# Kernel optimization log

Hardware: AMD Instinct MI355X
Metric: run time of the kernel (lower is better)

The kernel has to match this reference:

```python
import jax, jax.numpy as jnp
import numpy as np

N_NODES = 100000
N_EDGES = 3200000
D_IN = 128
D_HID = 128
N_CLASSES = 40


def setup_inputs() -> dict:
    key = jax.random.key(0)
    ks = jax.random.split(key, 8)
    x = jax.random.normal(ks[0], (N_NODES, D_IN), dtype=jnp.float32)
    edge_index = jax.random.randint(ks[1], (2, N_EDGES), 0, N_NODES, dtype=jnp.int64)
    s1 = 1.0 / np.sqrt(D_IN)
    s2 = 1.0 / np.sqrt(D_HID)
    W1 = jax.random.normal(ks[2], (D_IN, D_HID), dtype=jnp.float32) * s1
    b1 = jnp.zeros((D_HID,), dtype=jnp.float32)
    W2 = jax.random.normal(ks[3], (D_HID, D_HID), dtype=jnp.float32) * s2
    b2 = jnp.zeros((D_HID,), dtype=jnp.float32)
    Wl = jax.random.normal(ks[4], (D_HID, N_CLASSES), dtype=jnp.float32) * s2
    bl = jnp.zeros((N_CLASSES,), dtype=jnp.float32)
    return {"x": x, "edge_index": edge_index, "W1": W1, "b1": b1,
            "W2": W2, "b2": b2, "Wl": Wl, "bl": bl}


def _gcn_conv(x, W, b, src, dst, inv_sqrt_deg, n_nodes):
    # h = X @ W  (linear transform first: cheaper when out_dim <= in_dim)
    h = x @ W  # [N, d_out]
    # symmetric normalization: norm_e = deg(src)^-1/2 * deg(dst)^-1/2
    norm = inv_sqrt_deg[src] * inv_sqrt_deg[dst]  # [E]
    msg = h[src] * norm[:, None]                  # gather + scale  [E, d_out]
    out = jax.ops.segment_sum(msg, dst, num_segments=n_nodes)  # scatter-add
    return out + b


def reference(x, edge_index, W1, b1, W2, b2, Wl, bl):
    n = x.shape[0]
    # GCNConv adds self-loops before normalization (PyG default)
    loops = jnp.arange(n, dtype=edge_index.dtype)
    src = jnp.concatenate([edge_index[0], loops])
    dst = jnp.concatenate([edge_index[1], loops])
    deg = jax.ops.segment_sum(jnp.ones_like(dst, dtype=x.dtype), dst, num_segments=n)
    inv_sqrt_deg = jnp.where(deg > 0, jax.lax.rsqrt(deg), 0.0)

    h = _gcn_conv(x, W1, b1, src, dst, inv_sqrt_deg, n)
    h = jax.nn.relu(h)
    h = _gcn_conv(h, W2, b2, src, dst, inv_sqrt_deg, n)
    h = jax.nn.relu(h)
    return h @ Wl + bl
```

## Files before the change

### kernel.cpp

```cpp
#include <hip/hip_runtime.h>
#include <hip/hip_bf16.h>

typedef _Float16 f16;
typedef _Float16 f16x4 __attribute__((ext_vector_type(4)));
typedef _Float16 f16x8 __attribute__((ext_vector_type(8)));
typedef float f32x4 __attribute__((ext_vector_type(4)));

#define D 128
#define N_CLS 40
#define BN 128
#define NBMAX 1024


__global__ __launch_bounds__(256) void k_hist(const int* __restrict__ dst,
                                              int* __restrict__ bcnt, int e) {
  __shared__ int lh[NBMAX];
  for (int j = threadIdx.x; j < NBMAX; j += 256) lh[j] = 0;
  __syncthreads();
  int stride = gridDim.x * blockDim.x;
  for (int q = blockIdx.x * blockDim.x + threadIdx.x; q < e; q += stride)
    atomicAdd(&lh[dst[q] >> 7], 1);
  __syncthreads();
  for (int j = threadIdx.x; j < NBMAX; j += 256)
    if (lh[j]) atomicAdd(&bcnt[j], lh[j]);
}

__global__ __launch_bounds__(1024) void k_bscan(const int* __restrict__ bcnt,
                                                int* __restrict__ bbase,
                                                int* __restrict__ bcur) {
  __shared__ int sums[NBMAX];
  int t = threadIdx.x;
  int c = bcnt[t];
  sums[t] = c;
  __syncthreads();
  for (int off = 1; off < NBMAX; off <<= 1) {
    int a = (t >= off) ? sums[t - off] : 0;
    __syncthreads();
    sums[t] += a;
    __syncthreads();
  }
  bbase[t] = sums[t] - c;
  bcur[t] = sums[t] - c;
}

__global__ __launch_bounds__(256) void k_place(const int* __restrict__ src,
                                               const int* __restrict__ dst,
                                               int* __restrict__ bcur,
                                               unsigned int* __restrict__ binned,
                                               int e, int nwg) {
  __shared__ int lh[NBMAX];
  __shared__ int lofs[NBMAX];
  __shared__ int lcur[NBMAX];
  int chunk = (e + nwg - 1) / nwg;
  int lo = blockIdx.x * chunk;
  int hi = min(e, lo + chunk);
  int t = threadIdx.x;
  for (int j = t; j < NBMAX; j += 256) { lh[j] = 0; lcur[j] = 0; }
  __syncthreads();
  for (int q = lo + t; q < hi; q += 256) atomicAdd(&lh[dst[q] >> 7], 1);
  __syncthreads();
  for (int j = t; j < NBMAX; j += 256) {
    int c = lh[j];
    lofs[j] = c ? atomicAdd(&bcur[j], c) : 0;
  }
  __syncthreads();
  for (int q = lo + t; q < hi; q += 256) {
    int d = dst[q];
    int b = d >> 7;
    int r = atomicAdd(&lcur[b], 1);
    binned[lofs[b] + r] = ((unsigned int)(d & 127) << 17) | (unsigned int)src[q];
  }
}

__global__ __launch_bounds__(256) void k_csr(const unsigned int* __restrict__ binned,
                                             const int* __restrict__ bbase,
                                             int* __restrict__ csr,
                                             int* __restrict__ deg,
                                             float* __restrict__ isd,
                                             int* __restrict__ row_start, int n) {
  int b = blockIdx.x;
  int lo = bbase[b], hi = bbase[b + 1];
  __shared__ int h[BN];
  __shared__ int sc[BN];
  __shared__ int cur[BN];
  int t = threadIdx.x;
  if (t < BN) h[t] = 0;
  __syncthreads();
  for (int q = lo + t; q < hi; q += 256) atomicAdd(&h[binned[q] >> 17], 1);
  __syncthreads();
  if (t < BN) sc[t] = h[t];
  __syncthreads();
  for (int off = 1; off < BN; off <<= 1) {
    int a = 0;
    if (t < BN && t >= off) a = sc[t - off];
    __syncthreads();
    if (t < BN) sc[t] += a;
    __syncthreads();
  }
  if (t < BN) {
    int excl = sc[t] - h[t];
    cur[t] = lo + excl;
    int i = b * BN + t;
    if (i < n) {
      deg[i] = h[t];
      isd[i] = rsqrtf((float)(h[t] + 1));
      row_start[i] = lo + excl;
    }
  }
  __syncthreads();
  for (int q = lo + t; q < hi; q += 256) {
    unsigned int u = binned[q];
    int p = atomicAdd(&cur[u >> 17], 1);
    csr[p] = (int)(u & 0x1FFFF);
  }
}

template <bool HALF_IN>
__global__ __launch_bounds__(256) void k_gemm_m(const void* __restrict__ Xv,
                                                const float* __restrict__ W,
                                                const float* __restrict__ isd,
                                                f16* __restrict__ HS, int n) {
  __shared__ f16 At[64][136];
  __shared__ f16 Wt[128][136];
  const size_t ss = (size_t)n * 16;
  int t = threadIdx.x;
  int r0 = blockIdx.x * 64;
  if (!HALF_IN) {
    const float* X = (const float*)Xv;
    for (int q = t; q < 64 * 32; q += 256) {
      int row = q >> 5, cb = (q & 31) << 2;
      float4 v = {0.f, 0.f, 0.f, 0.f};
      if (r0 + row < n) v = *(const float4*)(X + (size_t)(r0 + row) * D + cb);
      f16x4 h = {(f16)v.x, (f16)v.y, (f16)v.z, (f16)v.w};
      *(f16x4*)&At[row][cb] = h;
    }
  } else {
    const f16* X = (const f16*)Xv;
    for (int q = t; q < 64 * 16; q += 256) {
      int row = q >> 4, cb = (q & 15) << 3;
      f16x8 v = 0;
      if (r0 + row < n) v = *(const f16x8*)(X + (size_t)(r0 + row) * D + cb);
      *(f16x8*)&At[row][cb] = v;
    }
  }
  for (int q = t; q < D * D; q += 256) {
    int k = q >> 7, c = q & 127;
    Wt[c][k] = (f16)W[q];
  }
  __syncthreads();

  int wave = t >> 6, lane = t & 63;
  int lw = lane & 15, kg = lane >> 4;
  f32x4 acc[8];
#pragma unroll
  for (int ct = 0; ct < 8; ++ct) acc[ct] = (f32x4)0.f;
#pragma unroll
  for (int ks = 0; ks < 4; ++ks) {
    f16x8 af = *(const f16x8*)&At[(wave << 4) + lw][ks * 32 + kg * 8];
#pragma unroll
    for (int ct = 0; ct < 8; ++ct) {
      f16x8 bf = *(const f16x8*)&Wt[ct * 16 + lw][ks * 32 + kg * 8];
      acc[ct] = __builtin_amdgcn_mfma_f32_16x16x32_f16(af, bf, acc[ct], 0, 0, 0);
    }
  }
  int rbase = r0 + (wave << 4) + (kg << 2);
  float sv[4];
#pragma unroll
  for (int rr = 0; rr < 4; ++rr)
    sv[rr] = (rbase + rr < n) ? isd[rbase + rr] : 0.f;
#pragma unroll
  for (int ct = 0; ct < 8; ++ct) {
#pragma unroll
    for (int rr = 0; rr < 4; ++rr) {
      int node = rbase + rr;
      if (node < n)
        HS[(size_t)ct * ss + (size_t)node * 16 + lw] = (f16)(acc[ct][rr] * sv[rr]);
    }
  }
}

__device__ inline f16x8 shfl_xor_f16x8(f16x8 v, int m) {
  union { f16x8 h; int i[4]; } u;
  u.h = v;
#pragma unroll
  for (int k = 0; k < 4; ++k) u.i[k] = __shfl_xor(u.i[k], m);
  return u.h;
}

__global__ __launch_bounds__(256) void k_aggs(const f16* __restrict__ HS,
                                              const int* __restrict__ csr,
                                              const int* __restrict__ row_start,
                                              const int* __restrict__ deg,
                                              const float* __restrict__ bias,
                                              f16* __restrict__ G, int n) {
  const size_t ss = (size_t)n * 16;
  int t = threadIdx.x;
  int wave = t >> 6, lane = t & 63;
  int g = lane >> 4, r = lane & 15;
  int s = blockIdx.x & 7;
  int i0 = ((blockIdx.x >> 3) << 4) + (wave << 2) + g;
  bool ok = i0 < n;
  int i = ok ? i0 : n - 1;
  int hf = r & 1, er = r >> 1;
  int dg = deg[i];
  const int* cp = csr + row_start[i];
  const char* sbase = (const char*)(HS + (size_t)s * ss);
  unsigned hofs = (unsigned)(hf << 4);
  f16x8 a0 = (f16x8)0, a1 = (f16x8)0;
  int iA = cp[er];
  int iB = cp[er + 8];
  for (int u = 0; u < dg; u += 16) {
    unsigned oA = ((unsigned)iA << 5) + hofs;
    unsigned oB = ((unsigned)iB << 5) + hofs;
    iA = cp[u + 16 + er];
    iB = cp[u + 24 + er];
    if (u + er < dg)
      a0 += *(const f16x8*)(sbase + oA);
    if (u + 8 + er < dg)
      a1 += *(const f16x8*)(sbase + oB);
  }
  f16x8 tv = a0 + a1;
  tv += shfl_xor_f16x8(tv, 2);
  tv += shfl_xor_f16x8(tv, 4);
  tv += shfl_xor_f16x8(tv, 8);
  f16x8 svv = *(const f16x8*)(sbase + ((unsigned)i << 5) + hofs);
  float di = rsqrtf((float)(dg + 1));
  const float* bp = bias + s * 16 + (hf << 3);
  float4 b0 = *(const float4*)bp;
  float4 b1 = *(const float4*)(bp + 4);
  float bv[8] = {b0.x, b0.y, b0.z, b0.w, b1.x, b1.y, b1.z, b1.w};
  f16x8 ov;
#pragma unroll
  for (int j = 0; j < 8; ++j) {
    float v = di * ((float)tv[j] + (float)svv[j]) + bv[j];
    v = v > 0.f ? v : 0.f;
    ov[j] = (f16)v;
  }
  if (ok && r < 2)
    *(f16x8*)(G + (size_t)i * D + s * 16 + (hf << 3)) = ov;
}

__global__ __launch_bounds__(256) void k_cls(const f16* __restrict__ H,
                                             const float* __restrict__ Wl,
                                             const float* __restrict__ bl,
                                             float* __restrict__ out, int n) {
  __shared__ float wt[N_CLS][D];
  int t = threadIdx.x;
  for (int q = t; q < D * N_CLS; q += 256) {
    int k = q / N_CLS, c = q - k * N_CLS;
    wt[c][k] = Wl[q];
  }
  int wv = t >> 6, lane = t & 63, g = lane >> 4, l = lane & 15;
  float bb0 = bl[l];
  float bb1 = bl[16 + l];
  float bb2 = (l < 8) ? bl[32 + l] : 0.f;
  __syncthreads();
  int node0 = (blockIdx.x << 7) + (wv << 2) + g;
  for (int it = 0; it < 8; ++it) {
    int node = node0 + it * 16;
    if (node >= n) break;
    f16x8 h = *(const f16x8*)(H + (size_t)node * D + l * 8);
    float hf[8];
#pragma unroll
    for (int j = 0; j < 8; ++j) hf[j] = (float)h[j];
    float r0 = bb0, r1 = bb1, r2 = bb2;
#pragma unroll 4
    for (int c = 0; c < N_CLS; ++c) {
      const float* wp = &wt[c][l * 8];
      float4 w0 = *(const float4*)wp;
      float4 w1 = *(const float4*)(wp + 4);
      float p = hf[0] * w0.x + hf[1] * w0.y + hf[2] * w0.z + hf[3] * w0.w +
                hf[4] * w1.x + hf[5] * w1.y + hf[6] * w1.z + hf[7] * w1.w;
      p += __shfl_xor(p, 1);
      p += __shfl_xor(p, 2);
      p += __shfl_xor(p, 4);
      p += __shfl_xor(p, 8);
      if ((c & 15) == l) {
        if (c < 16) r0 += p;
        else if (c < 32) r1 += p;
        else r2 += p;
      }
    }
    float* op = out + (size_t)node * N_CLS;
    op[l] = r0;
    op[16 + l] = r1;
    if (l < 8) op[32 + l] = r2;
  }
}

extern "C" void kernel_launch(void* const* d_in, const int* in_sizes, int n_in,
                              void* d_out, int out_size, void* d_ws, size_t ws_size,
                              hipStream_t stream) {
  const float* x  = (const float*)d_in[0];
  const int*   ei = (const int*)d_in[1];
  const float* W1 = (const float*)d_in[2];
  const float* b1 = (const float*)d_in[3];
  const float* W2 = (const float*)d_in[4];
  const float* b2 = (const float*)d_in[5];
  const float* Wl = (const float*)d_in[6];
  const float* bl = (const float*)d_in[7];
  float* out = (float*)d_out;

  const int n = in_sizes[0] / D;
  const int e = in_sizes[1] / 2;
  const int* src = ei;
  const int* dst = ei + e;
  const int nb = (n + BN - 1) / BN;

  char* ws = (char*)d_ws;
  size_t off = 0;
  auto alloc = [&](size_t bytes) -> void* {
    void* p = ws + off;
    off += (bytes + 255) & ~(size_t)255;
    return p;
  };
  int*   bcnt      = (int*)alloc(NBMAX * 4);
  int*   bbase     = (int*)alloc(NBMAX * 4);
  int*   bcur      = (int*)alloc(NBMAX * 4);
  int*   deg       = (int*)alloc((size_t)n * 4);
  int*   row_start = (int*)alloc((size_t)n * 4);
  float* isd       = (float*)alloc((size_t)n * 4);
  int*   csr       = (int*)alloc(((size_t)e + 64) * 4);
  f16*   hA        = (f16*)alloc((size_t)n * D * 2);
  f16*   hB        = (f16*)alloc((size_t)n * D * 2);
  unsigned int* binned = (unsigned int*)hA;

  hipMemsetAsync(bcnt, 0, NBMAX * 4, stream);
  hipMemsetAsync(csr + e, 0, 64 * 4, stream);

  const int nwg_place = 512;
  k_hist<<<1024, 256, 0, stream>>>(dst, bcnt, e);
  k_bscan<<<1, 1024, 0, stream>>>(bcnt, bbase, bcur);
  k_place<<<nwg_place, 256, 0, stream>>>(src, dst, bcur, binned, e, nwg_place);
  k_csr<<<nb, 256, 0, stream>>>(binned, bbase, csr, deg, isd, row_start, n);

  int gblocks = (n + 63) / 64;
  int ablocks = ((n + 15) / 16) * 8;
  k_gemm_m<false><<<gblocks, 256, 0, stream>>>(x, W1, isd, hA, n);
  k_aggs<<<ablocks, 256, 0, stream>>>(hA, csr, row_start, deg, b1, hB, n);
  k_gemm_m<true><<<gblocks, 256, 0, stream>>>(hB, W2, isd, hA, n);
  k_aggs<<<ablocks, 256, 0, stream>>>(hA, csr, row_start, deg, b2, hB, n);
  k_cls<<<(n + 127) / 128, 256, 0, stream>>>(hB, Wl, bl, out, n);
}
```

Measured before the change: 657.9 us.

## Widen feature slabs from 16 to 32 columns for aggregation gathers

The intermediate feature matrix is re-laid out as four slabs of 32 half-precision columns (64-byte rows) instead of eight slabs of 16 columns. Aggregation blocks now cover one of four slabs, so each edge gather fetches 64 bytes and the CSR index list is read half as many times across slabs. Each 16-lane group now handles four edges per step with four accumulators, and one cross-lane shuffle stage is dropped. The weight load in the GEMM is also vectorised to float4 reads. The trade-off is that each slab is larger, so it fits less well in L2 during the random gathers.

After: 646.3 us. No clear change (-1.8%).

```diff
diff --git a/kernel.cpp b/kernel.cpp
--- a/kernel.cpp
+++ b/kernel.cpp
@@ -122,7 +122,7 @@
                                                 f16* __restrict__ HS, int n) {
   __shared__ f16 At[64][136];
   __shared__ f16 Wt[128][136];
-  const size_t ss = (size_t)n * 16;
+  const size_t ss = (size_t)n * 32;
   int t = threadIdx.x;
   int r0 = blockIdx.x * 64;
   if (!HALF_IN) {
@@ -143,9 +143,13 @@
       *(f16x8*)&At[row][cb] = v;
     }
   }
-  for (int q = t; q < D * D; q += 256) {
-    int k = q >> 7, c = q & 127;
-    Wt[c][k] = (f16)W[q];
+  for (int q = t; q < (D * D) / 4; q += 256) {
+    int k = q >> 5, cq = (q & 31) << 2;
+    float4 w = *(const float4*)(W + (size_t)k * D + cq);
+    Wt[cq + 0][k] = (f16)w.x;
+    Wt[cq + 1][k] = (f16)w.y;
+    Wt[cq + 2][k] = (f16)w.z;
+    Wt[cq + 3][k] = (f16)w.w;
   }
   __syncthreads();
 
@@ -174,7 +178,8 @@
     for (int rr = 0; rr < 4; ++rr) {
       int node = rbase + rr;
       if (node < n)
-        HS[(size_t)ct * ss + (size_t)node * 16 + lw] = (f16)(acc[ct][rr] * sv[rr]);
+        HS[(size_t)(ct >> 1) * ss + (size_t)node * 32 + ((ct & 1) << 4) + lw] =
+            (f16)(acc[ct][rr] * sv[rr]);
     }
   }
 }
@@ -193,39 +198,48 @@
                                               const int* __restrict__ deg,
                                               const float* __restrict__ bias,
                                               f16* __restrict__ G, int n) {
-  const size_t ss = (size_t)n * 16;
+  const size_t ss = (size_t)n * 32;
   int t = threadIdx.x;
   int wave = t >> 6, lane = t & 63;
   int g = lane >> 4, r = lane & 15;
-  int s = blockIdx.x & 7;
-  int i0 = ((blockIdx.x >> 3) << 4) + (wave << 2) + g;
+  int s = blockIdx.x & 3;
+  int i0 = ((blockIdx.x >> 2) << 4) + (wave << 2) + g;
   bool ok = i0 < n;
   int i = ok ? i0 : n - 1;
-  int hf = r & 1, er = r >> 1;
+  int q = r & 3, er = r >> 2;
   int dg = deg[i];
   const int* cp = csr + row_start[i];
   const char* sbase = (const char*)(HS + (size_t)s * ss);
-  unsigned hofs = (unsigned)(hf << 4);
-  f16x8 a0 = (f16x8)0, a1 = (f16x8)0;
+  unsigned qofs = (unsigned)(q << 4);
+  f16x8 a0 = (f16x8)0, a1 = (f16x8)0, a2 = (f16x8)0, a3 = (f16x8)0;
   int iA = cp[er];
-  int iB = cp[er + 8];
+  int iB = cp[er + 4];
+  int iC = cp[er + 8];
+  int iD = cp[er + 12];
   for (int u = 0; u < dg; u += 16) {
-    unsigned oA = ((unsigned)iA << 5) + hofs;
-    unsigned oB = ((unsigned)iB << 5) + hofs;
+    unsigned oA = ((unsigned)iA << 6) + qofs;
+    unsigned oB = ((unsigned)iB << 6) + qofs;
+    unsigned oC = ((unsigned)iC << 6) + qofs;
+    unsigned oD = ((unsigned)iD << 6) + qofs;
     iA = cp[u + 16 + er];
-    iB = cp[u + 24 + er];
+    iB = cp[u + 20 + er];
+    iC = cp[u + 24 + er];
+    iD = cp[u + 28 + er];
     if (u + er < dg)
       a0 += *(const f16x8*)(sbase + oA);
+    if (u + 4 + er < dg)
+      a1 += *(const f16x8*)(sbase + oB);
     if (u + 8 + er < dg)
-      a1 += *(const f16x8*)(sbase + oB);
-  }
-  f16x8 tv = a0 + a1;
-  tv += shfl_xor_f16x8(tv, 2);
+      a2 += *(const f16x8*)(sbase + oC);
+    if (u + 12 + er < dg)
+      a3 += *(const f16x8*)(sbase + oD);
+  }
+  f16x8 tv = (a0 + a1) + (a2 + a3);
   tv += shfl_xor_f16x8(tv, 4);
   tv += shfl_xor_f16x8(tv, 8);
-  f16x8 svv = *(const f16x8*)(sbase + ((unsigned)i << 5) + hofs);
+  f16x8 svv = *(const f16x8*)(sbase + ((unsigned)i << 6) + qofs);
   float di = rsqrtf((float)(dg + 1));
-  const float* bp = bias + s * 16 + (hf << 3);
+  const float* bp = bias + s * 32 + (q << 3);
   float4 b0 = *(const float4*)bp;
   float4 b1 = *(const float4*)(bp + 4);
   float bv[8] = {b0.x, b0.y, b0.z, b0.w, b1.x, b1.y, b1.z, b1.w};
@@ -236,8 +250,8 @@
     v = v > 0.f ? v : 0.f;
     ov[j] = (f16)v;
   }
-  if (ok && r < 2)
-    *(f16x8*)(G + (size_t)i * D + s * 16 + (hf << 3)) = ov;
+  if (ok && er == 0)
+    *(f16x8*)(G + (size_t)i * D + s * 32 + (q << 3)) = ov;
 }
 
 __global__ __launch_bounds__(256) void k_cls(const f16* __restrict__ H,
@@ -335,7 +349,7 @@
   k_csr<<<nb, 256, 0, stream>>>(binned, bbase, csr, deg, isd, row_start, n);
 
   int gblocks = (n + 63) / 64;
-  int ablocks = ((n + 15) / 16) * 8;
+  int ablocks = ((n + 15) / 16) * 4;
   k_gemm_m<false><<<gblocks, 256, 0, stream>>>(x, W1, isd, hA, n);
   k_aggs<<<ablocks, 256, 0, stream>>>(hA, csr, row_start, deg, b1, hB, n);
   k_gemm_m<true><<<gblocks, 256, 0, stream>>>(hB, W2, isd, hA, n);
```
